# Kernel optimization log

Hardware: AMD Instinct MI355X
Metric: run time of the kernel (lower is better)

The kernel has to match this reference:

```python
import jax, jax.numpy as jnp
import numpy as np

B, C, M, NH, F_, W = 2, 8, 8, 8, 1024, 512  # batch, channels, attention_maps, heads, features, frames
HD = F_ // NH
EXP = 4


def _conv(x, w, b):
    y = jax.lax.conv_general_dilated(x, w, (1, 1), 'SAME',
                                     dimension_numbers=('NCHW', 'OIHW', 'NCHW'))
    return y + b[None, :, None, None]


def _rope(x):
    # x: (..., seq, d); lucidrains-style interleaved rotary embedding
    d, n = x.shape[-1], x.shape[-2]
    inv = 1.0 / (10000.0 ** (jnp.arange(0, d, 2, dtype=jnp.float32) / d))
    fr = jnp.repeat(jnp.arange(n, dtype=jnp.float32)[:, None] * inv[None, :], 2, axis=-1)
    cos, sin = jnp.cos(fr), jnp.sin(fr)
    xr = jnp.stack((-x[..., 1::2], x[..., 0::2]), axis=-1).reshape(x.shape)
    return x * cos + xr * sin


def _mcln(x, w, b, eps=1e-5):
    # MultichannelLayerNorm: normalize over features axis (axis=2 of B,C,F,W)
    mu = jnp.mean(x, axis=2, keepdims=True)
    var = jnp.var(x, axis=2, keepdims=True)
    return (x - mu) / jnp.sqrt(var + eps) * w[None, :, :, None] + b[None, :, :, None]


def _mclin(x, w_pw):
    # MultichannelLinear positionwise: per-channel matmul over features
    return jnp.einsum('bcfw,cgf->bcgw', x, w_pw)


def setup_inputs() -> dict:
    key = jax.random.key(0)
    ks = jax.random.split(key, 24)
    s = 0.02
    d = {
        'x': jax.random.normal(ks[0], (B, C, F_, W), jnp.float32),
        'prev_qk': jax.random.normal(ks[1], (B, M, NH, W, W), jnp.float32),
        'qconv_w': jax.random.normal(ks[2], (M, C, 3, 3), jnp.float32) * s,
        'qconv_b': jnp.zeros((M,), jnp.float32),
        'q_pw': jax.random.normal(ks[3], (M, F_, F_), jnp.float32) * s,
        'kconv_w': jax.random.normal(ks[4], (M, C, 3, 3), jnp.float32) * s,
        'kconv_b': jnp.zeros((M,), jnp.float32),
        'k_pw': jax.random.normal(ks[5], (M, F_, F_), jnp.float32) * s,
        'vconv_w': jax.random.normal(ks[6], (M, C, 3, 3), jnp.float32) * s,
        'vconv_b': jnp.zeros((M,), jnp.float32),
        'v_pw': jax.random.normal(ks[7], (M, F_, F_), jnp.float32) * s,
        'o_pw': jax.random.normal(ks[8], (M, F_, F_), jnp.float32) * s,
        'o_dw': jax.random.normal(ks[9], (M, M), jnp.float32) * s,
        'oproj_w': jax.random.normal(ks[10], (C, C + M, 3, 3), jnp.float32) * s,
        'oproj_b': jnp.zeros((C,), jnp.float32),
        'n1_w': jnp.ones((C, F_), jnp.float32),
        'n1_b': jnp.zeros((C, F_), jnp.float32),
        'c1_w': jax.random.normal(ks[11], (C * EXP, C, 3, 3), jnp.float32) * s,
        'c1_b': jnp.zeros((C * EXP,), jnp.float32),
        'c2_w': jax.random.normal(ks[12], (C, C * EXP, 3, 3), jnp.float32) * s,
        'c2_b': jnp.zeros((C,), jnp.float32),
        'n2_w': jnp.ones((C, F_), jnp.float32),
        'n2_b': jnp.zeros((C, F_), jnp.float32),
    }
    return d


def _encoder(x, prev_qk, qconv_w, qconv_b, q_pw, kconv_w, kconv_b, k_pw,
             vconv_w, vconv_b, v_pw, o_pw, o_dw, oproj_w, oproj_b,
             n1_w, n1_b, c1_w, c1_b, c2_w, c2_b, n2_w, n2_b):
    b, c, h, w = x.shape

    def heads(y):  # (B,M,F,W) -> (B,M,NH,W,HD)
        return y.transpose(0, 1, 3, 2).reshape(b, M, w, NH, HD).transpose(0, 1, 3, 2, 4)

    q = _rope(heads(_mclin(_conv(x, qconv_w, qconv_b), q_pw)))
    k = _rope(heads(_mclin(_conv(x, kconv_w, kconv_b), k_pw)))
    v = heads(_mclin(_conv(x, vconv_w, vconv_b), v_pw))

    qk = jnp.einsum('bmnqd,bmnkd->bmnqk', q, k) / jnp.sqrt(jnp.float32(h))
    qk = qk + prev_qk
    a = jnp.einsum('bmnqk,bmnkd->bmnqd', jax.nn.softmax(qk, axis=-1), v)
    a = a.transpose(0, 1, 3, 2, 4).reshape(b, M, w, NH * HD).transpose(0, 1, 3, 2)  # (B,M,F,W)
    a = jnp.einsum('bcfw,dc->bdfw', _mclin(a, o_pw), o_dw)  # depthwise o_linear
    z = _conv(jnp.concatenate((x, a), axis=1), oproj_w, oproj_b)

    hid = _mcln(x + z, n1_w, n1_b)  # dropout is identity in eval
    z2 = _conv(jax.nn.gelu(_conv(hid, c1_w, c1_b), approximate=False), c2_w, c2_b)
    out = _mcln(hid + z2, n2_w, n2_b)
    return out, qk


def reference(x, prev_qk, qconv_w, qconv_b, q_pw, kconv_w, kconv_b, k_pw,
              vconv_w, vconv_b, v_pw, o_pw, o_dw, oproj_w, oproj_b,
              n1_w, n1_b, c1_w, c1_b, c2_w, c2_b, n2_w, n2_b):
    out, qk = _encoder(x, prev_qk, qconv_w, qconv_b, q_pw, kconv_w, kconv_b, k_pw,
                       vconv_w, vconv_b, v_pw, o_pw, o_dw, oproj_w, oproj_b,
                       n1_w, n1_b, c1_w, c1_b, c2_w, c2_b, n2_w, n2_b)
    return (out, out, qk)
```

## Files before the change

### kernel.cpp

```cpp
#include <hip/hip_runtime.h>
#include <math.h>

#define B_ 2
#define C_ 8
#define M_ 8
#define NH_ 8
#define F_ 1024
#define W_ 512
#define HD_ 128
#define FW 524288L
#define PF_ 1026
#define PW_ 514

typedef __bf16 bf16_t;
typedef __bf16 bf16x8 __attribute__((ext_vector_type(8)));
typedef __bf16 bf16x4 __attribute__((ext_vector_type(4)));
typedef float f32x4 __attribute__((ext_vector_type(4)));

__device__ __forceinline__ void gload16(const void* g, void* l) {
    __builtin_amdgcn_global_load_lds(
        (const __attribute__((address_space(1))) unsigned int*)g,
        (__attribute__((address_space(3))) unsigned int*)l,
        16, 0, 0);
}

__device__ __forceinline__ float gelu_f(float v) {
    return 0.5f * v * (1.0f + erff(v * 0.70710678118f));
}

__device__ __forceinline__ void xcd_swz3(int& bx, int& by, int& bz) {
    const int nwg = gridDim.x * gridDim.y * gridDim.z;
    int orig = blockIdx.x + gridDim.x * (blockIdx.y + gridDim.y * blockIdx.z);
    orig = (orig & 7) * (nwg >> 3) + (orig >> 3);
    bx = orig % gridDim.x;
    int t = orig / gridDim.x;
    by = t % gridDim.y;
    bz = t / gridDim.y;
}

__global__ __launch_bounds__(256)
void cvtw_k(const float* __restrict__ qw, const float* __restrict__ kw,
            const float* __restrict__ vw, const float* __restrict__ ow,
            bf16_t* __restrict__ W4)
{
    long i = (long)blockIdx.x * 256 + threadIdx.x;
    const int wsel = (int)(i >> 21);
    const long off = i & 2097151L;
    const float* src = (wsel == 0) ? qw : (wsel == 1) ? kw : (wsel == 2) ? vw : ow;
    float4 v = ((const float4*)src)[off];
    bf16x4 r = { (bf16_t)v.x, (bf16_t)v.y, (bf16_t)v.z, (bf16_t)v.w };
    *(bf16x4*)&W4[i * 4] = r;
}

__global__ __launch_bounds__(256)
void pad_stage_k(const float* __restrict__ x, bf16_t* __restrict__ px)
{
    long i = (long)blockIdx.x * 256 + threadIdx.x;
    if (i >= (long)B_ * PF_ * PW_) return;
    int wc = (int)(i % PW_);
    long t = i / PW_;
    int fr = (int)(t % PF_);
    int b  = (int)(t / PF_);
    bf16x8 v = {};
    if (fr >= 1 && fr <= F_ && wc >= 1 && wc <= W_) {
        const float* s = x + (long)b * 8 * FW + (long)(fr - 1) * W_ + (wc - 1);
        #pragma unroll
        for (int c = 0; c < 8; ++c) v[c] = (bf16_t)s[c * FW];
    }
    *(bf16x8*)&px[i * 8] = v;
}

__global__ __launch_bounds__(256)
void borderz_all_k(bf16_t* __restrict__ p8a, bf16_t* __restrict__ p8b, bf16_t* __restrict__ p32)
{
    int i = blockIdx.x * 256 + threadIdx.x;
    if (i >= 2 * 3076) return;
    int b = i / 3076, p = i % 3076;
    int fr, wc;
    if (p < 514)       { fr = 0;    wc = p; }
    else if (p < 1028) { fr = 1025; wc = p - 514; }
    else if (p < 2052) { fr = 1 + (p - 1028); wc = 0; }
    else               { fr = 1 + (p - 2052); wc = 513; }
    long pix = ((long)b * PF_ + fr) * PW_ + wc;
    bf16x8 z = {};
    *(bf16x8*)&p8a[pix * 8] = z;
    *(bf16x8*)&p8b[pix * 8] = z;
    #pragma unroll
    for (int k = 0; k < 4; ++k) *(bf16x8*)&p32[pix * 32 + k * 8] = z;
}

__global__ void aprep_k(const float* __restrict__ qw, const float* __restrict__ kw,
                        const float* __restrict__ vw, const float* __restrict__ ow,
                        const float* __restrict__ c1w, const float* __restrict__ c2w,
                        const float* __restrict__ qb, const float* __restrict__ kb,
                        const float* __restrict__ vb,
                        bf16_t* __restrict__ a_qkv, bf16_t* __restrict__ a_op,
                        bf16_t* __restrict__ a_c1, bf16_t* __restrict__ a_c2,
                        float* __restrict__ bias_qkv)
{
    int mode = blockIdx.y;
    int i = blockIdx.x * 256 + threadIdx.x;
    if (mode == 0) {
        if (i < 3072) {
            int k = i & 31, co = (i >> 5) & 31, df = i >> 10;
            int tap = k >> 3, ci = k & 7;
            float v = 0.f;
            if (tap < 3) {
                if (co < 8)       v = qw[((co * 8 + ci) * 3 + df) * 3 + tap];
                else if (co < 16) v = kw[(((co - 8) * 8 + ci) * 3 + df) * 3 + tap];
                else if (co < 24) v = vw[(((co - 16) * 8 + ci) * 3 + df) * 3 + tap];
            }
            a_qkv[i] = (bf16_t)v;
        }
        if (i < 32) bias_qkv[i] = (i < 8) ? qb[i] : (i < 16) ? kb[i - 8] : (i < 24) ? vb[i - 16] : 0.f;
    } else if (mode == 1) {
        if (i < 3072) {
            int k = i & 63, co = (i >> 6) & 15, df = i >> 10;
            int src = k >> 5, r = k & 31, tap = r >> 3, ci = src * 8 + (r & 7);
            float v = 0.f;
            if (co < 8 && tap < 3) v = ow[((co * 16 + ci) * 3 + df) * 3 + tap];
            a_op[i] = (bf16_t)v;
        }
    } else if (mode == 2) {
        if (i < 3072) {
            int k = i & 31, co = (i >> 5) & 31, df = i >> 10;
            int tap = k >> 3, ci = k & 7;
            float v = (tap < 3) ? c1w[((co * 8 + ci) * 3 + df) * 3 + tap] : 0.f;
            a_c1[i] = (bf16_t)v;
        }
    } else {
        if (i < 4608) {
            int k = i % 96, co = (i / 96) & 15, df = i / (96 * 16);
            int tap = k >> 5, ci = k & 31;
            float v = (co < 8) ? c2w[((co * 32 + ci) * 3 + df) * 3 + tap] : 0.f;
            a_c2[i] = (bf16_t)v;
        }
    }
}

template<int CIN, int KSTEPS, int MFRAGS, int DUAL, int EPI>
__global__ __launch_bounds__(256)
void convg_k(const bf16_t* __restrict__ px0, const bf16_t* __restrict__ px1,
             const bf16_t* __restrict__ Ab, const float* __restrict__ bias,
             const float* __restrict__ resid, void* __restrict__ outp)
{
    const int f = blockIdx.y, b = blockIdx.z;
    const int tid = threadIdx.x, lane = tid & 63, wid = tid >> 6;
    const int l15 = lane & 15, l4 = lane >> 4;
    const int wbase = blockIdx.x * 256 + wid * 64;
    const int KW = KSTEPS * 32, M16 = MFRAGS * 16;

    bf16x8 af[3][MFRAGS][KSTEPS];
    #pragma unroll
    for (int df = 0; df < 3; ++df)
        #pragma unroll
        for (int mf = 0; mf < MFRAGS; ++mf)
            #pragma unroll
            for (int kk = 0; kk < KSTEPS; ++kk)
                af[df][mf][kk] = *(const bf16x8*)&Ab[(long)(df * M16 + mf * 16 + l15) * KW + kk * 32 + l4 * 8];

    f32x4 acc[MFRAGS][4];
    #pragma unroll
    for (int mf = 0; mf < MFRAGS; ++mf)
        #pragma unroll
        for (int nf = 0; nf < 4; ++nf)
            acc[mf][nf] = (f32x4){0.f, 0.f, 0.f, 0.f};

    #pragma unroll
    for (int df = 0; df < 3; ++df) {
        const long rowb = ((long)(b * PF_ + f + df)) * PW_ * CIN;
        #pragma unroll
        for (int nf = 0; nf < 4; ++nf) {
            const int wp = wbase + nf * 16 + l15;
            #pragma unroll
            for (int kk = 0; kk < KSTEPS; ++kk) {
                const bf16_t* src = (DUAL && kk == 1) ? px1 : px0;
                long addr = (CIN == 8) ? rowb + (long)(wp + l4) * 8
                                       : rowb + (long)(wp + kk) * 32 + l4 * 8;
                bf16x8 bv = *(const bf16x8*)&src[addr];
                #pragma unroll
                for (int mf = 0; mf < MFRAGS; ++mf)
                    acc[mf][nf] = __builtin_amdgcn_mfma_f32_16x16x32_bf16(
                        af[df][mf][kk], bv, acc[mf][nf], 0, 0, 0);
            }
        }
    }

    #pragma unroll
    for (int mf = 0; mf < MFRAGS; ++mf) {
        #pragma unroll
        for (int nf = 0; nf < 4; ++nf) {
            const int wp = wbase + nf * 16 + l15;
            if (EPI == 2) {
                const int cob = mf * 16 + l4 * 4;
                bf16x4 ov;
                #pragma unroll
                for (int r = 0; r < 4; ++r)
                    ov[r] = (bf16_t)gelu_f(acc[mf][nf][r] + bias[cob + r]);
                *(bf16x4*)&((bf16_t*)outp)[(((long)(b * PF_ + f + 1)) * PW_ + wp + 1) * 32 + cob] = ov;
            } else {
                #pragma unroll
                for (int r = 0; r < 4; ++r) {
                    const int co = mf * 16 + l4 * 4 + r;
                    float v = acc[mf][nf][r];
                    if (EPI == 0) {
                        if (co < 24)
                            ((bf16_t*)outp)[((long)(b * 24 + co)) * FW + (long)f * W_ + wp] = (bf16_t)(v + bias[co]);
                    } else {
                        if (co < 8) {
                            long oi = ((long)(b * 8 + co)) * FW + (long)f * W_ + wp;
                            ((bf16_t*)outp)[oi] = (bf16_t)(v + bias[co] + resid[oi]);
                        }
                    }
                }
            }
        }
    }
}

template<int EPI, int OUTBF>
__global__ __launch_bounds__(256, 4)
void gemm_mfma_k(const bf16_t* __restrict__ Ab, const bf16_t* __restrict__ Bb,
                 void* __restrict__ Cb, const float* __restrict__ Addb,
                 float scale, int Kdim, int lda, int ldb, int ldc,
                 long sA, long sB, long sC_hi, long sC_lo, int zdivC,
                 long sAdd, int aMod)
{
    __shared__ bf16_t sAt[8192];
    __shared__ bf16_t sBt[8192];

    int bx, by, bz;
    xcd_swz3(bx, by, bz);
    const int z = bz;
    const int m0 = by * 128;
    const int n0 = bx * 128;
    const int tid = threadIdx.x;
    const int lane = tid & 63, wid = tid >> 6;
    const int wr = (wid >> 1) * 64, wc = (wid & 1) * 64;
    const int l15 = lane & 15, l4 = lane >> 4;

    const bf16_t* A = Ab + (long)(z % aMod) * sA;
    const bf16_t* B = Bb + (long)z * sB;

    f32x4 acc[4][4];
    #pragma unroll
    for (int m = 0; m < 4; ++m)
        #pragma unroll
        for (int n = 0; n < 4; ++n)
            acc[m][n] = (f32x4){0.f, 0.f, 0.f, 0.f};

    const int grow = wid * 8 + (lane >> 3);
    const int gslot = lane & 7;

    for (int k0 = 0; k0 < Kdim; k0 += 64) {
        __syncthreads();
        #pragma unroll
        for (int r = 0; r < 4; ++r) {
            const int row = r * 32 + grow;
            gload16(A + (long)(m0 + row) * lda + k0 + ((gslot ^ (row & 7)) << 3),
                    sAt + r * 2048 + wid * 512);
        }
        #pragma unroll
        for (int r = 0; r < 4; ++r) {
            const int row = r * 32 + grow;
            gload16(B + (long)(n0 + row) * ldb + k0 + ((gslot ^ (row & 7)) << 3),
                    sBt + r * 2048 + wid * 512);
        }
        __syncthreads();

        bf16x8 afr[4][2], bfr[4][2];
        #pragma unroll
        for (int m = 0; m < 4; ++m) {
            const int row = wr + m * 16 + l15, swz = row & 7;
            afr[m][0] = *(const bf16x8*)&sAt[row * 64 + ((l4 ^ swz) << 3)];
            afr[m][1] = *(const bf16x8*)&sAt[row * 64 + (((4 + l4) ^ swz) << 3)];
        }
        #pragma unroll
        for (int n = 0; n < 4; ++n) {
            const int row = wc + n * 16 + l15, swz = row & 7;
            bfr[n][0] = *(const bf16x8*)&sBt[row * 64 + ((l4 ^ swz) << 3)];
            bfr[n][1] = *(const bf16x8*)&sBt[row * 64 + (((4 + l4) ^ swz) << 3)];
        }
        #pragma unroll
        for (int kk = 0; kk < 2; ++kk)
            #pragma unroll
            for (int m = 0; m < 4; ++m)
                #pragma unroll
                for (int n = 0; n < 4; ++n)
                    acc[m][n] = __builtin_amdgcn_mfma_f32_16x16x32_bf16(
                        afr[m][kk], bfr[n][kk], acc[m][n], 0, 0, 0);
    }

    const long zc = (long)(z / zdivC) * sC_hi + (long)(z % zdivC) * sC_lo;
    #pragma unroll
    for (int m = 0; m < 4; ++m) {
        #pragma unroll
        for (int n = 0; n < 4; ++n) {
            #pragma unroll
            for (int r = 0; r < 4; ++r) {
                int row = m0 + wr + m * 16 + l4 * 4 + r;
                int col = n0 + wc + n * 16 + l15;
                float v = acc[m][n][r];
                if (EPI == 1) v = v * scale + Addb[(long)z * sAdd + (long)row * ldc + col];
                long cidx = zc + (long)row * ldc + col;
                if (OUTBF) ((bf16_t*)Cb)[cidx] = (bf16_t)v;
                else       ((float*)Cb)[cidx]  = v;
            }
        }
    }
}

__global__ __launch_bounds__(256, 4)
void qkvgemm_k(const bf16_t* __restrict__ W4, const bf16_t* __restrict__ XT,
               bf16_t* __restrict__ outp )
{
    __shared__ bf16_t sAt[8192];
    __shared__ bf16_t sBt[8192];

    int bx, by, bz;
    xcd_swz3(bx, by, bz);
    const int zz = bz;
    const int path = zz >> 4, bm = zz & 15;
    const bf16_t* A = W4 + (long)(path * 8 + (bm & 7)) * 1048576L;
    const bf16_t* B = XT + (long)zz * FW;
    const int m0 = by * 128;
    const int n0 = bx * 128;
    const int tid = threadIdx.x;
    const int lane = tid & 63, wid = tid >> 6;
    const int wr = (wid >> 1) * 64, wc = (wid & 1) * 64;
    const int l15 = lane & 15, l4 = lane >> 4;

    f32x4 acc[4][4];
    #pragma unroll
    for (int m = 0; m < 4; ++m)
        #pragma unroll
        for (int n = 0; n < 4; ++n)
            acc[m][n] = (f32x4){0.f, 0.f, 0.f, 0.f};

    const int grow = wid * 8 + (lane >> 3);
    const int gslot = lane & 7;

    for (int k0 = 0; k0 < 1024; k0 += 64) {
        __syncthreads();
        #pragma unroll
        for (int r = 0; r < 4; ++r) {
            const int row = r * 32 + grow;
            gload16(A + (long)(m0 + row) * 1024 + k0 + ((gslot ^ (row & 7)) << 3),
                    sAt + r * 2048 + wid * 512);
        }
        #pragma unroll
        for (int r = 0; r < 4; ++r) {
            const int row = r * 32 + grow;
            gload16(B + (long)(n0 + row) * 1024 + k0 + ((gslot ^ (row & 7)) << 3),
                    sBt + r * 2048 + wid * 512);
        }
        __syncthreads();

        bf16x8 afr[4][2], bfr[4][2];
        #pragma unroll
        for (int m = 0; m < 4; ++m) {
            const int row = wr + m * 16 + l15, swz = row & 7;
            afr[m][0] = *(const bf16x8*)&sAt[row * 64 + ((l4 ^ swz) << 3)];
            afr[m][1] = *(const bf16x8*)&sAt[row * 64 + (((4 + l4) ^ swz) << 3)];
        }
        #pragma unroll
        for (int n = 0; n < 4; ++n) {
            const int row = wc + n * 16 + l15, swz = row & 7;
            bfr[n][0] = *(const bf16x8*)&sBt[row * 64 + ((l4 ^ swz) << 3)];
            bfr[n][1] = *(const bf16x8*)&sBt[row * 64 + (((4 + l4) ^ swz) << 3)];
        }
        #pragma unroll
        for (int kk = 0; kk < 2; ++kk)
            #pragma unroll
            for (int m = 0; m < 4; ++m)
                #pragma unroll
                for (int n = 0; n < 4; ++n)
                    acc[m][n] = __builtin_amdgcn_mfma_f32_16x16x32_bf16(
                        afr[m][kk], bfr[n][kk], acc[m][n], 0, 0, 0);
    }

    if (path < 2) {
        const long base = (long)path * 8388608L + (((long)bm * 8 + by) * 512L) * 128L;
        #pragma unroll
        for (int m = 0; m < 4; ++m) {
            const int d0 = wr + m * 16 + l4 * 4;
            const float inv0 = __expf(-(float)(d0 >> 1) * 0.14391156507f);
            const float inv1 = __expf(-(float)((d0 >> 1) + 1) * 0.14391156507f);
            #pragma unroll
            for (int n = 0; n < 4; ++n) {
                const int col = n0 + wc + n * 16 + l15;
                float s0, c0, s1, c1;
                __sincosf((float)col * inv0, &s0, &c0);
                __sincosf((float)col * inv1, &s1, &c1);
                float v0 = acc[m][n][0], v1 = acc[m][n][1];
                float v2 = acc[m][n][2], v3 = acc[m][n][3];
                bf16x4 ov = { (bf16_t)(v0 * c0 - v1 * s0), (bf16_t)(v1 * c0 + v0 * s0),
                              (bf16_t)(v2 * c1 - v3 * s1), (bf16_t)(v3 * c1 + v2 * s1) };
                *(bf16x4*)&outp[base + (long)col * 128 + d0] = ov;
            }
        }
    } else {
        const long base = 16777216L + (long)bm * FW;
        #pragma unroll
        for (int m = 0; m < 4; ++m)
            #pragma unroll
            for (int n = 0; n < 4; ++n)
                #pragma unroll
                for (int r = 0; r < 4; ++r) {
                    int row = m0 + wr + m * 16 + l4 * 4 + r;
                    int col = n0 + wc + n * 16 + l15;
                    outp[base + (long)row * 512 + col] = (bf16_t)acc[m][n][r];
                }
    }
}

__global__ __launch_bounds__(256, 4)
void smpv_k(const float* __restrict__ S, const bf16_t* __restrict__ VL,
            bf16_t* __restrict__ AT)
{
    __shared__ bf16_t sP[8192];
    __shared__ bf16_t sB[8192];
    __shared__ float smax[128], sinv[128];

    int bx, by, bz;
    xcd_swz3(bx, by, bz);
    const int z = bz;
    const int m0 = bx * 128;
    const float* Sb = S + (long)z * 262144L;
    const bf16_t* Bb = VL + (long)z * 65536L;
    const int tid = threadIdx.x, lane = tid & 63, wid = tid >> 6;
    const int l15 = lane & 15, l4 = lane >> 4;
    const int wr = (wid >> 1) * 64, wc = (wid & 1) * 64;

    {
        const int g = lane >> 4;
        for (int i = 0; i < 8; ++i) {
            const int row = i * 16 + wid * 4 + g;
            const float4* sr = (const float4*)(Sb + (long)(m0 + row) * 512);
            float4 v[8];
            #pragma unroll
            for (int j = 0; j < 8; ++j) v[j] = sr[l15 + j * 16];
            float mx = -1e30f;
            #pragma unroll
            for (int j = 0; j < 8; ++j)
                mx = fmaxf(mx, fmaxf(fmaxf(v[j].x, v[j].y), fmaxf(v[j].z, v[j].w)));
            #pragma unroll
            for (int o = 1; o <= 8; o <<= 1) mx = fmaxf(mx, __shfl_xor(mx, o, 64));
            float s = 0.f;
            #pragma unroll
            for (int j = 0; j < 8; ++j)
                s += __expf(v[j].x - mx) + __expf(v[j].y - mx) +
                     __expf(v[j].z - mx) + __expf(v[j].w - mx);
            #pragma unroll
            for (int o = 1; o <= 8; o <<= 1) s += __shfl_xor(s, o, 64);
            if (l15 == 0) { smax[row] = mx; sinv[row] = 1.0f / s; }
        }
    }
    __syncthreads();

    f32x4 acc[4][4];
    #pragma unroll
    for (int m = 0; m < 4; ++m)
        #pragma unroll
        for (int n = 0; n < 4; ++n)
            acc[m][n] = (f32x4){0.f, 0.f, 0.f, 0.f};

    const int grow = wid * 8 + (lane >> 3);
    const int gslot = lane & 7;
    const int prow0 = tid >> 4, pl = tid & 15;

    for (int kt = 0; kt < 512; kt += 64) {
        __syncthreads();
        #pragma unroll
        for (int p = 0; p < 8; ++p) {
            const int row = p * 16 + prow0;
            float4 v = *(const float4*)(Sb + (long)(m0 + row) * 512 + kt + pl * 4);
            float mr = smax[row];
            bf16x4 e = { (bf16_t)__expf(v.x - mr), (bf16_t)__expf(v.y - mr),
                         (bf16_t)__expf(v.z - mr), (bf16_t)__expf(v.w - mr) };
            *(bf16x4*)((char*)sP + row * 128 + ((((pl >> 1) ^ (row & 7))) << 4) + (pl & 1) * 8) = e;
        }
        #pragma unroll
        for (int r = 0; r < 4; ++r) {
            const int row = r * 32 + grow;
            gload16(Bb + (long)row * 512 + kt + ((gslot ^ (row & 7)) << 3),
                    sB + r * 2048 + wid * 512);
        }
        __syncthreads();

        bf16x8 afr[4][2], bfr[4][2];
        #pragma unroll
        for (int m = 0; m < 4; ++m) {
            const int row = wr + m * 16 + l15, swz = row & 7;
            afr[m][0] = *(const bf16x8*)&sP[row * 64 + ((l4 ^ swz) << 3)];
            afr[m][1] = *(const bf16x8*)&sP[row * 64 + (((4 + l4) ^ swz) << 3)];
        }
        #pragma unroll
        for (int n = 0; n < 4; ++n) {
            const int row = wc + n * 16 + l15, swz = row & 7;
            bfr[n][0] = *(const bf16x8*)&sB[row * 64 + ((l4 ^ swz) << 3)];
            bfr[n][1] = *(const bf16x8*)&sB[row * 64 + (((4 + l4) ^ swz) << 3)];
        }
        #pragma unroll
        for (int kk = 0; kk < 2; ++kk)
            #pragma unroll
            for (int m = 0; m < 4; ++m)
                #pragma unroll
                for (int n = 0; n < 4; ++n)
                    acc[m][n] = __builtin_amdgcn_mfma_f32_16x16x32_bf16(
                        afr[m][kk], bfr[n][kk], acc[m][n], 0, 0, 0);
    }

    const long base = (long)(z >> 3) * FW + (long)(z & 7) * 128L;
    #pragma unroll
    for (int m = 0; m < 4; ++m) {
        #pragma unroll
        for (int n = 0; n < 4; ++n) {
            #pragma unroll
            for (int r = 0; r < 4; ++r) {
                const int row = wr + m * 16 + l4 * 4 + r;
                const int col = wc + n * 16 + l15;
                float v = acc[m][n][r] * sinv[row];
                AT[base + (long)(m0 + row) * 1024 + col] = (bf16_t)v;
            }
        }
    }
}

__global__ __launch_bounds__(256)
void tcvt_k(const bf16_t* __restrict__ in, bf16_t* __restrict__ outp)
{
    __shared__ float tile[32][33];
    const int w0 = blockIdx.x * 32, f0 = blockIdx.y * 32;
    const int z = blockIdx.z;
    const int path = z >> 4, bm = z & 15;
    const int inSlice = (bm >> 3) * 24 + path * 8 + (bm & 7);
    const long ibase = (long)inSlice * FW;
    const long obase = (long)z * FW;
    const int tx = threadIdx.x & 31, ty = threadIdx.x >> 5;
    #pragma unroll
    for (int i = 0; i < 4; ++i)
        tile[ty + i * 8][tx] = (float)in[ibase + (long)(f0 + ty + i * 8) * W_ + w0 + tx];
    __syncthreads();
    #pragma unroll
    for (int i = 0; i < 4; ++i)
        outp[obase + (long)(w0 + ty + i * 8) * F_ + f0 + tx] = (bf16_t)tile[tx][ty + i * 8];
}

__global__ __launch_bounds__(256)
void odw_k(const bf16_t* __restrict__ t, const float* __restrict__ dw, bf16_t* __restrict__ px)
{
    long i = (long)blockIdx.x * 256 + threadIdx.x;
    int w = (int)(i & (W_ - 1));
    long q = i >> 9;
    int f = (int)(q & (F_ - 1));
    int b = (int)(q >> 10);
    const bf16_t* s = t + (long)b * 8 * FW + (long)f * W_ + w;
    float tv[8];
    #pragma unroll
    for (int c = 0; c < 8; ++c) tv[c] = (float)s[c * FW];
    bf16x8 o;
    #pragma unroll
    for (int d = 0; d < 8; ++d) {
        float a = 0.f;
        #pragma unroll
        for (int c = 0; c < 8; ++c) a += tv[c] * dw[d * 8 + c];
        o[d] = (bf16_t)a;
    }
    *(bf16x8*)&px[(((long)b * PF_ + f + 1) * PW_ + w + 1) * 8] = o;
}

template<typename TIN>
__global__ __launch_bounds__(256)
void mcln_k(const TIN* __restrict__ in, const float* __restrict__ gam,
            const float* __restrict__ bet, float* __restrict__ o1, float* __restrict__ o2,
            bf16_t* __restrict__ px)
{
    int wi = threadIdx.x & 31, fg = threadIdx.x >> 5;
    int w0 = blockIdx.x * 32;
    int c = blockIdx.y, b = blockIdx.z;
    long base = ((long)b * C_ + c) * FW + w0 + wi;
    float s = 0.f, q = 0.f;
    for (int f = fg; f < F_; f += 8) {
        float v = (float)in[base + (long)f * W_];
        s += v; q += v * v;
    }
    __shared__ float rs[8][33], rq[8][33];
    __shared__ float mu_s[32], inv_s[32];
    rs[fg][wi] = s; rq[fg][wi] = q;
    __syncthreads();
    if (fg == 0) {
        float ts = 0.f, tq = 0.f;
        for (int g = 0; g < 8; ++g) { ts += rs[g][wi]; tq += rq[g][wi]; }
        float mu = ts * (1.0f / F_);
        float var = tq * (1.0f / F_) - mu * mu;
        mu_s[wi] = mu;
        inv_s[wi] = rsqrtf(var + 1e-5f);
    }
    __syncthreads();
    float mu = mu_s[wi], inv = inv_s[wi];
    for (int f = fg; f < F_; f += 8) {
        float v = (float)in[base + (long)f * W_];
        float r = (v - mu) * inv * gam[c * F_ + f] + bet[c * F_ + f];
        long oi = base + (long)f * W_;
        o1[oi] = r;
        if (o2) o2[oi] = r;
        if (px) px[(((long)b * PF_ + f + 1) * PW_ + (w0 + wi) + 1) * 8 + c] = (bf16_t)r;
    }
}

extern "C" void kernel_launch(void* const* d_in, const int* in_sizes, int n_in,
                              void* d_out, int out_size, void* d_ws, size_t ws_size,
                              hipStream_t stream) {
    (void)in_sizes; (void)n_in; (void)out_size; (void)ws_size;
    const float* x        = (const float*)d_in[0];
    const float* prev_qk  = (const float*)d_in[1];
    const float* qconv_w  = (const float*)d_in[2];
    const float* qconv_b  = (const float*)d_in[3];
    const float* q_pw     = (const float*)d_in[4];
    const float* kconv_w  = (const float*)d_in[5];
    const float* kconv_b  = (const float*)d_in[6];
    const float* k_pw     = (const float*)d_in[7];
    const float* vconv_w  = (const float*)d_in[8];
    const float* vconv_b  = (const float*)d_in[9];
    const float* v_pw     = (const float*)d_in[10];
    const float* o_pw     = (const float*)d_in[11];
    const float* o_dw     = (const float*)d_in[12];
    const float* oproj_w  = (const float*)d_in[13];
    const float* oproj_b  = (const float*)d_in[14];
    const float* n1_w     = (const float*)d_in[15];
    const float* n1_b     = (const float*)d_in[16];
    const float* c1_w     = (const float*)d_in[17];
    const float* c1_b     = (const float*)d_in[18];
    const float* c2_w     = (const float*)d_in[19];
    const float* c2_b     = (const float*)d_in[20];
    const float* n2_w     = (const float*)d_in[21];
    const float* n2_b     = (const float*)d_in[22];

    float* out    = (float*)d_out;
    float* qk_out = out + 16777216L;

    char* wsb = (char*)d_ws;
    bf16_t* PX8  = (bf16_t*)(wsb + 0L);
    bf16_t* XT48 = (bf16_t*)(wsb + 16876032L);
    bf16_t* QR   = (bf16_t*)(wsb + 67207680L);
    bf16_t* KR   = (bf16_t*)(wsb + 83984896L);
    bf16_t* VL   = (bf16_t*)(wsb + 100762112L);
    bf16_t* QKV  = (bf16_t*)(wsb + 117539328L);
    bf16_t* AT   = (bf16_t*)(wsb + 117539328L);
    bf16_t* F1b  = (bf16_t*)(wsb + 134316544L);
    bf16_t* PXA2 = (bf16_t*)(wsb + 83984896L);
    float*  HID  = (float*) (wsb + 16876032L);
    bf16_t* PXC1 = (bf16_t*)(wsb + 50430464L);
    bf16_t* PRE  = (bf16_t*)(wsb + 151093760L);
    bf16_t* PXH  = (bf16_t*)(wsb + 167870976L);
    bf16_t* ABQ  = (bf16_t*)(wsb + 184748032L);
    bf16_t* ABO  = (bf16_t*)(wsb + 184748032L + 16384L);
    bf16_t* ABC1 = (bf16_t*)(wsb + 184748032L + 32768L);
    bf16_t* ABC2 = (bf16_t*)(wsb + 184748032L + 49152L);
    float*  BQKV = (float*) (wsb + 184748032L + 65536L);
    bf16_t* W4   = (bf16_t*)(wsb + 184879104L);

    const dim3 cvgrid(2, F_, B_);
    const dim3 tgrid(16, 32, 48);
    const long BIG = 1 << 30;

    cvtw_k<<<32768, 256, 0, stream>>>(q_pw, k_pw, v_pw, o_pw, W4);
    aprep_k<<<dim3(18, 4), 256, 0, stream>>>(qconv_w, kconv_w, vconv_w, oproj_w, c1_w, c2_w,
                                             qconv_b, kconv_b, vconv_b,
                                             ABQ, ABO, ABC1, ABC2, BQKV);
    pad_stage_k<<<4121, 256, 0, stream>>>(x, PX8);

    convg_k<8, 1, 2, 0, 0><<<cvgrid, 256, 0, stream>>>(PX8, nullptr, ABQ, BQKV, nullptr, QKV);

    tcvt_k<<<tgrid, 256, 0, stream>>>(QKV, XT48);
    qkvgemm_k<<<dim3(4, 8, 48), 256, 0, stream>>>(W4, XT48, QR);

    gemm_mfma_k<1, 0><<<dim3(4, 4, 128), 256, 0, stream>>>(QR, KR, qk_out, prev_qk,
        0.03125f, HD_, HD_, HD_, W_, 65536L, 65536L, 262144L, 0L, 1, 262144L, (int)BIG);
    smpv_k<<<dim3(4, 1, 128), 256, 0, stream>>>(qk_out, VL, AT);

    gemm_mfma_k<0, 1><<<dim3(4, 8, 16), 256, 0, stream>>>(W4 + 25165824L, AT, F1b, nullptr, 1.f,
        F_, F_, F_, W_, 1048576L, 524288L, 524288L, 0L, 1, 0L, 8);
    odw_k<<<4096, 256, 0, stream>>>(F1b, o_dw, PXA2);
    borderz_all_k<<<25, 256, 0, stream>>>(PXA2, PXH, PXC1);

    convg_k<8, 2, 1, 1, 1><<<cvgrid, 256, 0, stream>>>(PX8, PXA2, ABO, oproj_b, x, PRE);

    mcln_k<bf16_t><<<dim3(16, 8, 2), 256, 0, stream>>>(PRE, n1_w, n1_b, HID, nullptr, PXH);

    convg_k<8, 1, 2, 0, 2><<<cvgrid, 256, 0, stream>>>(PXH, nullptr, ABC1, c1_b, nullptr, PXC1);
    convg_k<32, 3, 1, 0, 1><<<cvgrid, 256, 0, stream>>>(PXC1, nullptr, ABC2, c2_b, HID, PRE);
    mcln_k<bf16_t><<<dim3(16, 8, 2), 256, 0, stream>>>(PRE, n2_w, n2_b, out, out + 8388608L, nullptr);
}
```

Measured before the change: 653.8 us.

## Fuse softmax row stats into QK GEMM, merge prep kernels, store hidden in bf16

A dedicated QK GEMM kernel now applies the scale and prev_qk add, then computes per-row partial max and exp-sum for each 128-column tile into a stats buffer. The softmax-PV kernel merges these partials instead of re-reading the full 512-wide score rows to find max and sum. Separately, the weight-convert, pad, conv-weight prep and border-zero kernels are merged into one launch. The post-norm hidden residual is also stored in bf16 instead of fp32, cutting traffic at the cost of residual precision.

```diff
diff --git a/kernel.cpp b/kernel.cpp
--- a/kernel.cpp
+++ b/kernel.cpp
@@ -39,110 +39,106 @@
 }
 
 __global__ __launch_bounds__(256)
-void cvtw_k(const float* __restrict__ qw, const float* __restrict__ kw,
+void prep_k(const float* __restrict__ q_pw, const float* __restrict__ k_pw,
+            const float* __restrict__ v_pw, const float* __restrict__ o_pw,
+            const float* __restrict__ x,
+            const float* __restrict__ qw, const float* __restrict__ kw,
             const float* __restrict__ vw, const float* __restrict__ ow,
-            bf16_t* __restrict__ W4)
-{
-    long i = (long)blockIdx.x * 256 + threadIdx.x;
-    const int wsel = (int)(i >> 21);
-    const long off = i & 2097151L;
-    const float* src = (wsel == 0) ? qw : (wsel == 1) ? kw : (wsel == 2) ? vw : ow;
-    float4 v = ((const float4*)src)[off];
-    bf16x4 r = { (bf16_t)v.x, (bf16_t)v.y, (bf16_t)v.z, (bf16_t)v.w };
-    *(bf16x4*)&W4[i * 4] = r;
-}
-
-__global__ __launch_bounds__(256)
-void pad_stage_k(const float* __restrict__ x, bf16_t* __restrict__ px)
-{
-    long i = (long)blockIdx.x * 256 + threadIdx.x;
-    if (i >= (long)B_ * PF_ * PW_) return;
-    int wc = (int)(i % PW_);
-    long t = i / PW_;
-    int fr = (int)(t % PF_);
-    int b  = (int)(t / PF_);
-    bf16x8 v = {};
-    if (fr >= 1 && fr <= F_ && wc >= 1 && wc <= W_) {
-        const float* s = x + (long)b * 8 * FW + (long)(fr - 1) * W_ + (wc - 1);
-        #pragma unroll
-        for (int c = 0; c < 8; ++c) v[c] = (bf16_t)s[c * FW];
-    }
-    *(bf16x8*)&px[i * 8] = v;
-}
-
-__global__ __launch_bounds__(256)
-void borderz_all_k(bf16_t* __restrict__ p8a, bf16_t* __restrict__ p8b, bf16_t* __restrict__ p32)
-{
-    int i = blockIdx.x * 256 + threadIdx.x;
-    if (i >= 2 * 3076) return;
-    int b = i / 3076, p = i % 3076;
-    int fr, wc;
-    if (p < 514)       { fr = 0;    wc = p; }
-    else if (p < 1028) { fr = 1025; wc = p - 514; }
-    else if (p < 2052) { fr = 1 + (p - 1028); wc = 0; }
-    else               { fr = 1 + (p - 2052); wc = 513; }
-    long pix = ((long)b * PF_ + fr) * PW_ + wc;
-    bf16x8 z = {};
-    *(bf16x8*)&p8a[pix * 8] = z;
-    *(bf16x8*)&p8b[pix * 8] = z;
-    #pragma unroll
-    for (int k = 0; k < 4; ++k) *(bf16x8*)&p32[pix * 32 + k * 8] = z;
-}
-
-__global__ void aprep_k(const float* __restrict__ qw, const float* __restrict__ kw,
-                        const float* __restrict__ vw, const float* __restrict__ ow,
-                        const float* __restrict__ c1w, const float* __restrict__ c2w,
-                        const float* __restrict__ qb, const float* __restrict__ kb,
-                        const float* __restrict__ vb,
-                        bf16_t* __restrict__ a_qkv, bf16_t* __restrict__ a_op,
-                        bf16_t* __restrict__ a_c1, bf16_t* __restrict__ a_c2,
-                        float* __restrict__ bias_qkv)
-{
-    int mode = blockIdx.y;
-    int i = blockIdx.x * 256 + threadIdx.x;
-    if (mode == 0) {
-        if (i < 3072) {
-            int k = i & 31, co = (i >> 5) & 31, df = i >> 10;
-            int tap = k >> 3, ci = k & 7;
-            float v = 0.f;
-            if (tap < 3) {
-                if (co < 8)       v = qw[((co * 8 + ci) * 3 + df) * 3 + tap];
-                else if (co < 16) v = kw[(((co - 8) * 8 + ci) * 3 + df) * 3 + tap];
-                else if (co < 24) v = vw[(((co - 16) * 8 + ci) * 3 + df) * 3 + tap];
-            }
-            a_qkv[i] = (bf16_t)v;
-        }
-        if (i < 32) bias_qkv[i] = (i < 8) ? qb[i] : (i < 16) ? kb[i - 8] : (i < 24) ? vb[i - 16] : 0.f;
-    } else if (mode == 1) {
-        if (i < 3072) {
-            int k = i & 63, co = (i >> 6) & 15, df = i >> 10;
-            int src = k >> 5, r = k & 31, tap = r >> 3, ci = src * 8 + (r & 7);
-            float v = 0.f;
-            if (co < 8 && tap < 3) v = ow[((co * 16 + ci) * 3 + df) * 3 + tap];
-            a_op[i] = (bf16_t)v;
-        }
-    } else if (mode == 2) {
-        if (i < 3072) {
-            int k = i & 31, co = (i >> 5) & 31, df = i >> 10;
-            int tap = k >> 3, ci = k & 7;
-            float v = (tap < 3) ? c1w[((co * 8 + ci) * 3 + df) * 3 + tap] : 0.f;
-            a_c1[i] = (bf16_t)v;
+            const float* __restrict__ c1w, const float* __restrict__ c2w,
+            const float* __restrict__ qb, const float* __restrict__ kb,
+            const float* __restrict__ vb,
+            bf16_t* __restrict__ W4, bf16_t* __restrict__ px,
+            bf16_t* __restrict__ a_qkv, bf16_t* __restrict__ a_op,
+            bf16_t* __restrict__ a_c1, bf16_t* __restrict__ a_c2,
+            float* __restrict__ bias_qkv,
+            bf16_t* __restrict__ p8a, bf16_t* __restrict__ p8b, bf16_t* __restrict__ p32)
+{
+    const int bid = blockIdx.x, tid = threadIdx.x;
+    if (bid < 32768) {
+        long i = (long)bid * 256 + tid;
+        const int wsel = (int)(i >> 21);
+        const long off = i & 2097151L;
+        const float* src = (wsel == 0) ? q_pw : (wsel == 1) ? k_pw : (wsel == 2) ? v_pw : o_pw;
+        float4 v = ((const float4*)src)[off];
+        bf16x4 r = { (bf16_t)v.x, (bf16_t)v.y, (bf16_t)v.z, (bf16_t)v.w };
+        *(bf16x4*)&W4[i * 4] = r;
+    } else if (bid < 36889) {
+        long i = (long)(bid - 32768) * 256 + tid;
+        if (i >= (long)B_ * PF_ * PW_) return;
+        int wc = (int)(i % PW_);
+        long t = i / PW_;
+        int fr = (int)(t % PF_);
+        int b  = (int)(t / PF_);
+        bf16x8 v = {};
+        if (fr >= 1 && fr <= F_ && wc >= 1 && wc <= W_) {
+            const float* s = x + (long)b * 8 * FW + (long)(fr - 1) * W_ + (wc - 1);
+            #pragma unroll
+            for (int c = 0; c < 8; ++c) v[c] = (bf16_t)s[c * FW];
+        }
+        *(bf16x8*)&px[i * 8] = v;
+    } else if (bid < 36961) {
+        int sub = bid - 36889;
+        int mode = sub / 18;
+        int i = (sub % 18) * 256 + tid;
+        if (mode == 0) {
+            if (i < 3072) {
+                int k = i & 31, co = (i >> 5) & 31, df = i >> 10;
+                int tap = k >> 3, ci = k & 7;
+                float v = 0.f;
+                if (tap < 3) {
+                    if (co < 8)       v = qw[((co * 8 + ci) * 3 + df) * 3 + tap];
+                    else if (co < 16) v = kw[(((co - 8) * 8 + ci) * 3 + df) * 3 + tap];
+                    else if (co < 24) v = vw[(((co - 16) * 8 + ci) * 3 + df) * 3 + tap];
+                }
+                a_qkv[i] = (bf16_t)v;
+            }
+            if (i < 32) bias_qkv[i] = (i < 8) ? qb[i] : (i < 16) ? kb[i - 8] : (i < 24) ? vb[i - 16] : 0.f;
+        } else if (mode == 1) {
+            if (i < 3072) {
+                int k = i & 63, co = (i >> 6) & 15, df = i >> 10;
+                int src = k >> 5, r = k & 31, tap = r >> 3, ci = src * 8 + (r & 7);
+                float v = 0.f;
+                if (co < 8 && tap < 3) v = ow[((co * 16 + ci) * 3 + df) * 3 + tap];
+                a_op[i] = (bf16_t)v;
+            }
+        } else if (mode == 2) {
+            if (i < 3072) {
+                int k = i & 31, co = (i >> 5) & 31, df = i >> 10;
+                int tap = k >> 3, ci = k & 7;
+                float v = (tap < 3) ? c1w[((co * 8 + ci) * 3 + df) * 3 + tap] : 0.f;
+                a_c1[i] = (bf16_t)v;
+            }
+        } else {
+            if (i < 4608) {
+                int k = i % 96, co = (i / 96) & 15, df = i / (96 * 16);
+                int tap = k >> 5, ci = k & 31;
+                float v = (co < 8) ? c2w[((co * 32 + ci) * 3 + df) * 3 + tap] : 0.f;
+                a_c2[i] = (bf16_t)v;
+            }
         }
     } else {
-        if (i < 4608) {
-            int k = i % 96, co = (i / 96) & 15, df = i / (96 * 16);
-            int tap = k >> 5, ci = k & 31;
-            float v = (co < 8) ? c2w[((co * 32 + ci) * 3 + df) * 3 + tap] : 0.f;
-            a_c2[i] = (bf16_t)v;
-        }
-    }
-}
-
-template<int CIN, int KSTEPS, int MFRAGS, int DUAL, int EPI>
+        int i = (bid - 36961) * 256 + tid;
+        if (i >= 2 * 3076) return;
+        int b = i / 3076, p = i % 3076;
+        int fr, wc;
+        if (p < 514)       { fr = 0;    wc = p; }
+        else if (p < 1028) { fr = 1025; wc = p - 514; }
+        else if (p < 2052) { fr = 1 + (p - 1028); wc = 0; }
+        else               { fr = 1 + (p - 2052); wc = 513; }
+        long pix = ((long)b * PF_ + fr) * PW_ + wc;
+        bf16x8 z = {};
+        *(bf16x8*)&p8a[pix * 8] = z;
+        *(bf16x8*)&p8b[pix * 8] = z;
+        #pragma unroll
+        for (int k = 0; k < 4; ++k) *(bf16x8*)&p32[pix * 32 + k * 8] = z;
+    }
+}
+
+template<int CIN, int KSTEPS, int MFRAGS, int DUAL, int EPI, int RESBF>
 __global__ __launch_bounds__(256)
 void convg_k(const bf16_t* __restrict__ px0, const bf16_t* __restrict__ px1,
              const bf16_t* __restrict__ Ab, const float* __restrict__ bias,
-             const float* __restrict__ resid, void* __restrict__ outp)
+             const void* __restrict__ resid, void* __restrict__ outp)
 {
     const int f = blockIdx.y, b = blockIdx.z;
     const int tid = threadIdx.x, lane = tid & 63, wid = tid >> 6;
@@ -209,7 +205,9 @@
                     } else {
                         if (co < 8) {
                             long oi = ((long)(b * 8 + co)) * FW + (long)f * W_ + wp;
-                            ((bf16_t*)outp)[oi] = (bf16_t)(v + bias[co] + resid[oi]);
+                            float rv = RESBF ? (float)((const bf16_t*)resid)[oi]
+                                             : ((const float*)resid)[oi];
+                            ((bf16_t*)outp)[oi] = (bf16_t)(v + bias[co] + rv);
                         }
                     }
                 }
@@ -218,13 +216,12 @@
     }
 }
 
-template<int EPI, int OUTBF>
+template<int OUTBF>
 __global__ __launch_bounds__(256, 4)
 void gemm_mfma_k(const bf16_t* __restrict__ Ab, const bf16_t* __restrict__ Bb,
-                 void* __restrict__ Cb, const float* __restrict__ Addb,
-                 float scale, int Kdim, int lda, int ldb, int ldc,
-                 long sA, long sB, long sC_hi, long sC_lo, int zdivC,
-                 long sAdd, int aMod)
+                 void* __restrict__ Cb,
+                 int Kdim, int lda, int ldb, int ldc,
+                 long sA, long sB, long sC_hi, long sC_lo, int zdivC, int aMod)
 {
     __shared__ bf16_t sAt[8192];
     __shared__ bf16_t sBt[8192];
@@ -301,12 +298,128 @@
                 int row = m0 + wr + m * 16 + l4 * 4 + r;
                 int col = n0 + wc + n * 16 + l15;
                 float v = acc[m][n][r];
-                if (EPI == 1) v = v * scale + Addb[(long)z * sAdd + (long)row * ldc + col];
                 long cidx = zc + (long)row * ldc + col;
                 if (OUTBF) ((bf16_t*)Cb)[cidx] = (bf16_t)v;
                 else       ((float*)Cb)[cidx]  = v;
             }
         }
+    }
+}
+
+__global__ __launch_bounds__(256)
+void qkgemm_k(const bf16_t* __restrict__ QR, const bf16_t* __restrict__ KR,
+              float* __restrict__ Cb, const float* __restrict__ prevb,
+              float* __restrict__ stats)
+{
+    __shared__ bf16_t sAt[8192];
+    __shared__ bf16_t sBt[8192];
+    __shared__ float red[2][128][2];
+
+    int bx, by, bz;
+    xcd_swz3(bx, by, bz);
+    const int z = bz;
+    const int m0 = by * 128;
+    const int n0 = bx * 128;
+    const int tid = threadIdx.x;
+    const int lane = tid & 63, wid = tid >> 6;
+    const int wr = (wid >> 1) * 64, wc = (wid & 1) * 64;
+    const int l15 = lane & 15, l4 = lane >> 4;
+
+    const bf16_t* A = QR + (long)z * 65536L;
+    const bf16_t* B = KR + (long)z * 65536L;
+
+    f32x4 acc[4][4];
+    #pragma unroll
+    for (int m = 0; m < 4; ++m)
+        #pragma unroll
+        for (int n = 0; n < 4; ++n)
+            acc[m][n] = (f32x4){0.f, 0.f, 0.f, 0.f};
+
+    const int grow = wid * 8 + (lane >> 3);
+    const int gslot = lane & 7;
+
+    for (int k0 = 0; k0 < 128; k0 += 64) {
+        __syncthreads();
+        #pragma unroll
+        for (int r = 0; r < 4; ++r) {
+            const int row = r * 32 + grow;
+            gload16(A + (long)(m0 + row) * 128 + k0 + ((gslot ^ (row & 7)) << 3),
+                    sAt + r * 2048 + wid * 512);
+        }
+        #pragma unroll
+        for (int r = 0; r < 4; ++r) {
+            const int row = r * 32 + grow;
+            gload16(B + (long)(n0 + row) * 128 + k0 + ((gslot ^ (row & 7)) << 3),
+                    sBt + r * 2048 + wid * 512);
+        }
+        __syncthreads();
+
+        bf16x8 afr[4][2], bfr[4][2];
+        #pragma unroll
+        for (int m = 0; m < 4; ++m) {
+            const int row = wr + m * 16 + l15, swz = row & 7;
+            afr[m][0] = *(const bf16x8*)&sAt[row * 64 + ((l4 ^ swz) << 3)];
+            afr[m][1] = *(const bf16x8*)&sAt[row * 64 + (((4 + l4) ^ swz) << 3)];
+        }
+        #pragma unroll
+        for (int n = 0; n < 4; ++n) {
+            const int row = wc + n * 16 + l15, swz = row & 7;
+            bfr[n][0] = *(const bf16x8*)&sBt[row * 64 + ((l4 ^ swz) << 3)];
+            bfr[n][1] = *(const bf16x8*)&sBt[row * 64 + (((4 + l4) ^ swz) << 3)];
+        }
+        #pragma unroll
+        for (int kk = 0; kk < 2; ++kk)
+            #pragma unroll
+            for (int m = 0; m < 4; ++m)
+                #pragma unroll
+                for (int n = 0; n < 4; ++n)
+                    acc[m][n] = __builtin_amdgcn_mfma_f32_16x16x32_bf16(
+                        afr[m][kk], bfr[n][kk], acc[m][n], 0, 0, 0);
+    }
+
+    const long zc = (long)z * 262144L;
+    #pragma unroll
+    for (int m = 0; m < 4; ++m) {
+        #pragma unroll
+        for (int n = 0; n < 4; ++n) {
+            #pragma unroll
+            for (int r = 0; r < 4; ++r) {
+                int row = m0 + wr + m * 16 + l4 * 4 + r;
+                int col = n0 + wc + n * 16 + l15;
+                float v = acc[m][n][r] * 0.03125f + prevb[zc + (long)row * 512 + col];
+                acc[m][n][r] = v;
+                Cb[zc + (long)row * 512 + col] = v;
+            }
+        }
+    }
+    #pragma unroll
+    for (int m = 0; m < 4; ++m) {
+        #pragma unroll
+        for (int r = 0; r < 4; ++r) {
+            float mx = -1e30f;
+            #pragma unroll
+            for (int n = 0; n < 4; ++n) mx = fmaxf(mx, acc[m][n][r]);
+            #pragma unroll
+            for (int o = 1; o <= 8; o <<= 1) mx = fmaxf(mx, __shfl_xor(mx, o, 64));
+            float se = 0.f;
+            #pragma unroll
+            for (int n = 0; n < 4; ++n) se += __expf(acc[m][n][r] - mx);
+            #pragma unroll
+            for (int o = 1; o <= 8; o <<= 1) se += __shfl_xor(se, o, 64);
+            if (l15 == 0) {
+                int row = wr + m * 16 + l4 * 4 + r;
+                red[wid & 1][row][0] = mx;
+                red[wid & 1][row][1] = se;
+            }
+        }
+    }
+    __syncthreads();
+    if (tid < 128) {
+        float ma = red[0][tid][0], sa = red[0][tid][1];
+        float mb = red[1][tid][0], sb = red[1][tid][1];
+        float M = fmaxf(ma, mb);
+        float S = sa * __expf(ma - M) + sb * __expf(mb - M);
+        *(float2*)&stats[(((long)z * 4 + bx) * 512 + m0 + tid) * 2] = make_float2(M, S);
     }
 }
 
@@ -416,7 +529,7 @@
 
 __global__ __launch_bounds__(256, 4)
 void smpv_k(const float* __restrict__ S, const bf16_t* __restrict__ VL,
-            bf16_t* __restrict__ AT)
+            const float* __restrict__ stats, bf16_t* __restrict__ AT)
 {
     __shared__ bf16_t sP[8192];
     __shared__ bf16_t sB[8192];
@@ -432,29 +545,17 @@
     const int l15 = lane & 15, l4 = lane >> 4;
     const int wr = (wid >> 1) * 64, wc = (wid & 1) * 64;
 
-    {
-        const int g = lane >> 4;
-        for (int i = 0; i < 8; ++i) {
-            const int row = i * 16 + wid * 4 + g;
-            const float4* sr = (const float4*)(Sb + (long)(m0 + row) * 512);
-            float4 v[8];
-            #pragma unroll
-            for (int j = 0; j < 8; ++j) v[j] = sr[l15 + j * 16];
-            float mx = -1e30f;
-            #pragma unroll
-            for (int j = 0; j < 8; ++j)
-                mx = fmaxf(mx, fmaxf(fmaxf(v[j].x, v[j].y), fmaxf(v[j].z, v[j].w)));
-            #pragma unroll
-            for (int o = 1; o <= 8; o <<= 1) mx = fmaxf(mx, __shfl_xor(mx, o, 64));
-            float s = 0.f;
-            #pragma unroll
-            for (int j = 0; j < 8; ++j)
-                s += __expf(v[j].x - mx) + __expf(v[j].y - mx) +
-                     __expf(v[j].z - mx) + __expf(v[j].w - mx);
-            #pragma unroll
-            for (int o = 1; o <= 8; o <<= 1) s += __shfl_xor(s, o, 64);
-            if (l15 == 0) { smax[row] = mx; sinv[row] = 1.0f / s; }
-        }
+    if (tid < 128) {
+        float M = -1e30f, Ssum = 0.f;
+        #pragma unroll
+        for (int kb = 0; kb < 4; ++kb) {
+            float2 p = *(const float2*)&stats[(((long)z * 4 + kb) * 512 + m0 + tid) * 2];
+            float nm = fmaxf(M, p.x);
+            Ssum = Ssum * __expf(M - nm) + p.y * __expf(p.x - nm);
+            M = nm;
+        }
+        smax[tid] = M;
+        sinv[tid] = 1.0f / Ssum;
     }
     __syncthreads();
 
@@ -570,10 +671,10 @@
     *(bf16x8*)&px[(((long)b * PF_ + f + 1) * PW_ + w + 1) * 8] = o;
 }
 
-template<typename TIN>
+template<typename TIN, int O1BF>
 __global__ __launch_bounds__(256)
 void mcln_k(const TIN* __restrict__ in, const float* __restrict__ gam,
-            const float* __restrict__ bet, float* __restrict__ o1, float* __restrict__ o2,
+            const float* __restrict__ bet, void* __restrict__ o1, float* __restrict__ o2,
             bf16_t* __restrict__ px)
 {
     int wi = threadIdx.x & 31, fg = threadIdx.x >> 5;
@@ -603,7 +704,8 @@
         float v = (float)in[base + (long)f * W_];
         float r = (v - mu) * inv * gam[c * F_ + f] + bet[c * F_ + f];
         long oi = base + (long)f * W_;
-        o1[oi] = r;
+        if (O1BF) ((bf16_t*)o1)[oi] = (bf16_t)r;
+        else      ((float*)o1)[oi]  = r;
         if (o2) o2[oi] = r;
         if (px) px[(((long)b * PF_ + f + 1) * PW_ + (w0 + wi) + 1) * 8 + c] = (bf16_t)r;
     }
@@ -642,54 +744,52 @@
 
     char* wsb = (char*)d_ws;
     bf16_t* PX8  = (bf16_t*)(wsb + 0L);
-    bf16_t* XT48 = (bf16_t*)(wsb + 16876032L);
-    bf16_t* QR   = (bf16_t*)(wsb + 67207680L);
-    bf16_t* KR   = (bf16_t*)(wsb + 83984896L);
-    bf16_t* VL   = (bf16_t*)(wsb + 100762112L);
-    bf16_t* QKV  = (bf16_t*)(wsb + 117539328L);
-    bf16_t* AT   = (bf16_t*)(wsb + 117539328L);
-    bf16_t* F1b  = (bf16_t*)(wsb + 134316544L);
-    bf16_t* PXA2 = (bf16_t*)(wsb + 83984896L);
-    float*  HID  = (float*) (wsb + 16876032L);
-    bf16_t* PXC1 = (bf16_t*)(wsb + 50430464L);
-    bf16_t* PRE  = (bf16_t*)(wsb + 151093760L);
-    bf16_t* PXH  = (bf16_t*)(wsb + 167870976L);
-    bf16_t* ABQ  = (bf16_t*)(wsb + 184748032L);
-    bf16_t* ABO  = (bf16_t*)(wsb + 184748032L + 16384L);
-    bf16_t* ABC1 = (bf16_t*)(wsb + 184748032L + 32768L);
-    bf16_t* ABC2 = (bf16_t*)(wsb + 184748032L + 49152L);
-    float*  BQKV = (float*) (wsb + 184748032L + 65536L);
-    bf16_t* W4   = (bf16_t*)(wsb + 184879104L);
+    bf16_t* W4   = (bf16_t*)(wsb + 16876032L);
+    bf16_t* QR   = (bf16_t*)(wsb + 83984896L);
+    bf16_t* KR   = (bf16_t*)(wsb + 100762112L);
+    bf16_t* VL   = (bf16_t*)(wsb + 117539328L);
+    bf16_t* XT48 = (bf16_t*)(wsb + 134316544L);
+    bf16_t* HIDb = (bf16_t*)(wsb + 134316544L);
+    bf16_t* QKV  = (bf16_t*)(wsb + 184648192L);
+    bf16_t* AT   = (bf16_t*)(wsb + 184648192L);
+    bf16_t* F1b  = (bf16_t*)(wsb + 201425408L);
+    bf16_t* PRE  = (bf16_t*)(wsb + 218202624L);
+    bf16_t* PXA2 = (bf16_t*)(wsb + 234979840L);
+    bf16_t* PXH  = (bf16_t*)(wsb + 251855616L);
+    bf16_t* PXC1 = (bf16_t*)(wsb + 268731392L);
+    bf16_t* ABQ  = (bf16_t*)(wsb + 336233984L);
+    bf16_t* ABO  = (bf16_t*)(wsb + 336233984L + 16384L);
+    bf16_t* ABC1 = (bf16_t*)(wsb + 336233984L + 32768L);
+    bf16_t* ABC2 = (bf16_t*)(wsb + 336233984L + 49152L);
+    float*  BQKV = (float*) (wsb + 336233984L + 65536L);
+    float*  STAT = (float*) (wsb + 336365056L);
 
     const dim3 cvgrid(2, F_, B_);
     const dim3 tgrid(16, 32, 48);
-    const long BIG = 1 << 30;
-
-    cvtw_k<<<32768, 256, 0, stream>>>(q_pw, k_pw, v_pw, o_pw, W4);
-    aprep_k<<<dim3(18, 4), 256, 0, stream>>>(qconv_w, kconv_w, vconv_w, oproj_w, c1_w, c2_w,
-                                             qconv_b, kconv_b, vconv_b,
-                                             ABQ, ABO, ABC1, ABC2, BQKV);
-    pad_stage_k<<<4121, 256, 0, stream>>>(x, PX8);
-
-    convg_k<8, 1, 2, 0, 0><<<cvgrid, 256, 0, stream>>>(PX8, nullptr, ABQ, BQKV, nullptr, QKV);
+
+    prep_k<<<36986, 256, 0, stream>>>(q_pw, k_pw, v_pw, o_pw, x,
+                                      qconv_w, kconv_w, vconv_w, oproj_w, c1_w, c2_w,
+                                      qconv_b, kconv_b, vconv_b,
+                                      W4, PX8, ABQ, ABO, ABC1, ABC2, BQKV,
+                                      PXA2, PXH, PXC1);
+
+    convg_k<8, 1, 2, 0, 0, 0><<<cvgrid, 256, 0, stream>>>(PX8, nullptr, ABQ, BQKV, nullptr, QKV);
 
     tcvt_k<<<tgrid, 256, 0, stream>>>(QKV, XT48);
     qkvgemm_k<<<dim3(4, 8, 48), 256, 0, stream>>>(W4, XT48, QR);
 
-    gemm_mfma_k<1, 0><<<dim3(4, 4, 128), 256, 0, stream>>>(QR, KR, qk_out, prev_qk,
-        0.03125f, HD_, HD_, HD_, W_, 65536L, 65536L, 262144L, 0L, 1, 262144L, (int)BIG);
-    smpv_k<<<dim3(4, 1, 128), 256, 0, stream>>>(qk_out, VL, AT);
-
-    gemm_mfma_k<0, 1><<<dim3(4, 8, 16), 256, 0, stream>>>(W4 + 25165824L, AT, F1b, nullptr, 1.f,
-        F_, F_, F_, W_, 1048576L, 524288L, 524288L, 0L, 1, 0L, 8);
+    qkgemm_k<<<dim3(4, 4, 128), 256, 0, stream>>>(QR, KR, qk_out, prev_qk, STAT);
+    smpv_k<<<dim3(4, 1, 128), 256, 0, stream>>>(qk_out, VL, STAT, AT);
+
+    gemm_mfma_k<1><<<dim3(4, 8, 16), 256, 0, stream>>>(W4 + 25165824L, AT, F1b,
+        F_, F_, F_, W_, 1048576L, 524288L, 524288L, 0L, 1, 8);
     odw_k<<<4096, 256, 0, stream>>>(F1b, o_dw, PXA2);
-    borderz_all_k<<<25, 256, 0, stream>>>(PXA2, PXH, PXC1);
-
-    convg_k<8, 2, 1, 1, 1><<<cvgrid, 256, 0, stream>>>(PX8, PXA2, ABO, oproj_b, x, PRE);
-
-    mcln_k<bf16_t><<<dim3(16, 8, 2), 256, 0, stream>>>(PRE, n1_w, n1_b, HID, nullptr, PXH);
-
-    convg_k<8, 1, 2, 0, 2><<<cvgrid, 256, 0, stream>>>(PXH, nullptr, ABC1, c1_b, nullptr, PXC1);
-    convg_k<32, 3, 1, 0, 1><<<cvgrid, 256, 0, stream>>>(PXC1, nullptr, ABC2, c2_b, HID, PRE);
-    mcln_k<bf16_t><<<dim3(16, 8, 2), 256, 0, stream>>>(PRE, n2_w, n2_b, out, out + 8388608L, nullptr);
-}
+
+    convg_k<8, 2, 1, 1, 1, 0><<<cvgrid, 256, 0, stream>>>(PX8, PXA2, ABO, oproj_b, x, PRE);
+
+    mcln_k<bf16_t, 1><<<dim3(16, 8, 2), 256, 0, stream>>>(PRE, n1_w, n1_b, HIDb, nullptr, PXH);
+
+    convg_k<8, 1, 2, 0, 2, 0><<<cvgrid, 256, 0, stream>>>(PXH, nullptr, ABC1, c1_b, nullptr, PXC1);
+    convg_k<32, 3, 1, 0, 1, 1><<<cvgrid, 256, 0, stream>>>(PXC1, nullptr, ABC2, c2_b, HIDb, PRE);
+    mcln_k<bf16_t, 0><<<dim3(16, 8, 2), 256, 0, stream>>>(PRE, n2_w, n2_b, out, out + 8388608L, nullptr);
+}
```

After: 653.7 us. Within noise of the previous version (-0.0%).
